# Kernel tuning notes

Measured on AMD Instinct MI355X. Metric: run time of the kernel, lower is better.

The kernel has to match this reference:

```python
import jax, jax.numpy as jnp
import numpy as np
import math

B, S, D, H = 4, 1024, 1024, 16

def setup_inputs() -> dict:
    key = jax.random.key(0)
    ks = jax.random.split(key, 9)
    Q = jax.random.normal(ks[0], (B, S, D), dtype=jnp.float32)
    K = jax.random.normal(ks[1], (B, S, D), dtype=jnp.float32)
    V = jax.random.normal(ks[2], (B, S, D), dtype=jnp.float32)
    mask = jax.random.randint(ks[3], (B, 1, S, S), 0, 2, dtype=jnp.int32)
    # keep the diagonal unmasked so no causal row is fully -inf (avoids NaN softmax rows)
    eye = jnp.eye(S, dtype=jnp.int32)[None, None]
    mask = jnp.maximum(mask, eye)
    sc = 1.0 / math.sqrt(D)
    Wq = jax.random.normal(ks[4], (D, D), dtype=jnp.float32) * sc
    Wk = jax.random.normal(ks[5], (D, D), dtype=jnp.float32) * sc
    Wv = jax.random.normal(ks[6], (D, D), dtype=jnp.float32) * sc
    Wo = jax.random.normal(ks[7], (D, D), dtype=jnp.float32) * sc
    bo = jnp.zeros((D,), dtype=jnp.float32)
    return {"Q": Q, "K": K, "V": V, "mask": mask,
            "Wq": Wq, "Wk": Wk, "Wv": Wv, "Wo": Wo, "bo": bo, "heads": H}


def reference(Q, K, V, mask, Wq, Wk, Wv, Wo, bo, heads):
    b, s, d = Q.shape
    dk = d // heads
    # QKV projections (bias-free) and head split: [B,S,D] -> [B,H,S,dk]
    def split_heads(x, W):
        return (x @ W).reshape(b, s, heads, dk).transpose(0, 2, 1, 3)
    q = split_heads(Q, Wq)
    k = split_heads(K, Wk)
    v = split_heads(V, Wv)
    # raw scores [B,H,S,S]
    attn = jnp.einsum('bhqd,bhkd->bhqk', q, k) / jnp.sqrt(jnp.float32(dk))
    # multiplicative padding mask
    attn = attn * mask.astype(attn.dtype)
    # sequential=True: torch.tril zeroes the strict upper triangle
    causal = jnp.tril(jnp.ones((s, s), dtype=attn.dtype))
    attn = attn * causal
    # the module's quirk: exact zeros become -inf before softmax
    attn = jnp.where(attn == 0, -jnp.inf, attn)
    scores = jax.nn.softmax(attn, axis=-1)  # dropout is identity in eval / p=0
    ctx = jnp.einsum('bhqk,bhkd->bhqd', scores, v)
    concat = ctx.transpose(0, 2, 1, 3).reshape(b, s, d)
    return concat @ Wo + bo
```

## Files before the change

### kernel.cpp

```cpp
#include <hip/hip_runtime.h>

#define DEV __device__ __forceinline__

typedef __bf16 bf16x8 __attribute__((ext_vector_type(8)));
typedef float f32x4 __attribute__((ext_vector_type(4)));
typedef unsigned short u16x8 __attribute__((ext_vector_type(8)));
typedef unsigned int u32;
typedef unsigned long long u64;

DEV unsigned short f2bf(float f) {
  union { float f; unsigned int u; } v; v.f = f;
  unsigned int r = v.u + 0x7fffu + ((v.u >> 16) & 1u);
  return (unsigned short)(r >> 16);
}

DEV int swz(int row, int kbyte) { return row * 128 + (kbyte ^ ((row & 7) << 4)); }

DEV void gload16(const void* g, void* l) {
  __builtin_amdgcn_global_load_lds(
      (const __attribute__((address_space(1))) unsigned int*)g,
      (__attribute__((address_space(3))) unsigned int*)l, 16, 0, 0);
}

__global__ __launch_bounds__(256) void pack_mask_k(const int* __restrict__ mask,
                                                   u32* __restrict__ bits) {
  int e = blockIdx.x * 256 + threadIdx.x;
  int k = e & 1023, q = (e >> 10) & 1023;
  int m = (mask[e] != 0) && (k <= q);
  unsigned long long b = __ballot(m);
  int lane = threadIdx.x & 63;
  if (lane == 0)       bits[e >> 5] = (u32)b;
  else if (lane == 32) bits[e >> 5] = (u32)(b >> 32);
}

__global__ __launch_bounds__(256) void xcast_k(
    const float* __restrict__ Qx, const float* __restrict__ Kx, const float* __restrict__ Vx,
    unsigned short* __restrict__ qp, unsigned short* __restrict__ kp,
    unsigned short* __restrict__ vp) {
  int z = blockIdx.y;
  const float* X = z == 0 ? Qx : z == 1 ? Kx : Vx;
  unsigned short* P = z == 0 ? qp : z == 1 ? kp : vp;
  int tile = blockIdx.x;
  int mb = tile >> 4, kt = tile & 15;
  int t = threadIdx.x;
  size_t tb = (size_t)tile * 16384;
  #pragma unroll
  for (int i = 0; i < 4; i++) {
    int idx = i * 256 + t;
    int r = idx >> 3, j = idx & 7;
    int c0 = ((j * 16) ^ ((r & 7) << 4)) >> 1;
    const float* src = X + (size_t)(mb * 128 + r) * 1024 + kt * 64 + c0;
    f32x4 a = *(const f32x4*)src;
    f32x4 bq = *(const f32x4*)(src + 4);
    u16x8 o;
    o[0] = f2bf(a[0]); o[1] = f2bf(a[1]); o[2] = f2bf(a[2]); o[3] = f2bf(a[3]);
    o[4] = f2bf(bq[0]); o[5] = f2bf(bq[1]); o[6] = f2bf(bq[2]); o[7] = f2bf(bq[3]);
    *(u16x8*)((char*)P + tb + (size_t)idx * 16) = o;
  }
}

__global__ __launch_bounds__(256) void wtrans_k(
    const float* __restrict__ W0, const float* __restrict__ W1,
    const float* __restrict__ W2, const float* __restrict__ W3,
    unsigned short* __restrict__ O0, unsigned short* __restrict__ O1,
    unsigned short* __restrict__ O2, unsigned short* __restrict__ O3) {
  const float* W = blockIdx.z == 0 ? W0 : blockIdx.z == 1 ? W1 : blockIdx.z == 2 ? W2 : W3;
  unsigned short* O = blockIdx.z == 0 ? O0 : blockIdx.z == 1 ? O1 : blockIdx.z == 2 ? O2 : O3;
  __shared__ float tile[32][33];
  int tx = threadIdx.x, ty = threadIdx.y;
  int x0 = blockIdx.x * 32, y0 = blockIdx.y * 32;
  #pragma unroll
  for (int i = 0; i < 4; i++)
    tile[ty + i * 8][tx] = W[(size_t)(y0 + ty + i * 8) * 1024 + x0 + tx];
  __syncthreads();
  #pragma unroll
  for (int i = 0; i < 4; i++) {
    int n = x0 + ty + i * 8, k = y0 + tx;
    size_t a = (size_t)((n >> 7) * 16 + (k >> 6)) * 16384 + swz(n & 127, (k & 63) * 2);
    *(unsigned short*)((char*)O + a) = f2bf(tile[tx][ty + i * 8]);
  }
}

__global__ __launch_bounds__(256) void proj_gemm_k(
    const unsigned short* __restrict__ Qp, const unsigned short* __restrict__ Kp,
    const unsigned short* __restrict__ Vp,
    const unsigned short* __restrict__ Wtq, const unsigned short* __restrict__ Wtk,
    const unsigned short* __restrict__ Wtv,
    unsigned short* __restrict__ qo, unsigned short* __restrict__ ko,
    unsigned short* __restrict__ vo) {
  int z = blockIdx.z;
  const unsigned short* Ap = z == 0 ? Qp : z == 1 ? Kp : Vp;
  const unsigned short* Bp = z == 0 ? Wtq : z == 1 ? Wtk : Wtv;
  unsigned short* out = z == 0 ? qo : z == 1 ? ko : vo;

  __shared__ __align__(16) unsigned short As[8192];
  __shared__ __align__(16) unsigned short Bs[8192];

  int t = threadIdx.x, w = t >> 6, lane = t & 63;
  int wm = (w >> 1) * 64, wn = (w & 1) * 64;
  int rl = lane & 15, kgrp = lane >> 4;

  f32x4 acc[4][4];
  #pragma unroll
  for (int m = 0; m < 4; m++)
    #pragma unroll
    for (int n = 0; n < 4; n++)
      #pragma unroll
      for (int r = 0; r < 4; r++) acc[m][n][r] = 0.f;

  for (int kt = 0; kt < 16; kt++) {
    __syncthreads();
    const char* ab = (const char*)Ap + (size_t)(blockIdx.x * 16 + kt) * 16384 + w * 1024 + lane * 16;
    const char* bb = (const char*)Bp + (size_t)(blockIdx.y * 16 + kt) * 16384 + w * 1024 + lane * 16;
    char* al = (char*)As + w * 1024;
    char* bl = (char*)Bs + w * 1024;
    #pragma unroll
    for (int i = 0; i < 4; i++) {
      gload16(ab + i * 4096, al + i * 4096);
      gload16(bb + i * 4096, bl + i * 4096);
    }
    __syncthreads();
    #pragma unroll
    for (int kk = 0; kk < 2; kk++) {
      bf16x8 af[4], bfr[4];
      #pragma unroll
      for (int m = 0; m < 4; m++)
        af[m] = *(const bf16x8*)((const char*)As + swz(wm + m * 16 + rl, kk * 64 + kgrp * 16));
      #pragma unroll
      for (int n = 0; n < 4; n++)
        bfr[n] = *(const bf16x8*)((const char*)Bs + swz(wn + n * 16 + rl, kk * 64 + kgrp * 16));
      #pragma unroll
      for (int m = 0; m < 4; m++)
        #pragma unroll
        for (int n = 0; n < 4; n++)
          acc[m][n] = __builtin_amdgcn_mfma_f32_16x16x32_bf16(af[m], bfr[n], acc[m][n], 0, 0, 0);
    }
  }
  int m0 = blockIdx.x * 128, n0 = blockIdx.y * 128;
  #pragma unroll
  for (int m = 0; m < 4; m++)
    #pragma unroll
    for (int n = 0; n < 4; n++)
      #pragma unroll
      for (int r = 0; r < 4; r++) {
        int grow = m0 + wm + m * 16 + kgrp * 4 + r;
        int gcol = n0 + wn + n * 16 + rl;
        int b = grow >> 10, s = grow & 1023;
        int h = gcol >> 6, d = gcol & 63;
        unsigned short val = f2bf(acc[m][n][r]);
        if (z == 0) {
          out[(size_t)((b * 16 + h) * 1024 + s) * 64 + d] = val;
        } else if (z == 1) {
          *(unsigned short*)((char*)out +
            (size_t)((b * 16 + h) * 16 + (s >> 6)) * 8192 + swz(s & 63, d * 2)) = val;
        } else {
          *(unsigned short*)((char*)out +
            (size_t)((b * 16 + h) * 16 + (s >> 6)) * 8192 + swz(d, (s & 63) * 2)) = val;
        }
      }
}

__global__ __launch_bounds__(256) void attn_k(
    const unsigned short* __restrict__ qg, const unsigned short* __restrict__ kp,
    const unsigned short* __restrict__ vp, const u32* __restrict__ mbits,
    unsigned short* __restrict__ ccp) {
  int p = blockIdx.x;
  int bh = blockIdx.y;
  int b = bh >> 4, h = bh & 15;
  int t = threadIdx.x, w = t >> 6, lane = t & 63;
  int rl = lane & 15, kgrp = lane >> 4;

  const int qtA = p, qtB = 15 - p, J = qtB + 1;
  const int q0s[2] = {qtA * 64, qtB * 64};

  __shared__ __align__(16) unsigned short Ks[2][4096];
  __shared__ __align__(16) unsigned short Vs[2][4096];
  __shared__ __align__(16) unsigned short Ps[4][1024];

  const size_t qoff = (size_t)bh * 65536;
  const char* kbase = (const char*)kp + (size_t)bh * 131072;
  const char* vbase = (const char*)vp + (size_t)bh * 131072;

  bf16x8 qa[2][2];
  #pragma unroll
  for (int tl = 0; tl < 2; tl++) {
    int row = q0s[tl] + w * 16 + rl;
    #pragma unroll
    for (int kk = 0; kk < 2; kk++)
      qa[tl][kk] = *(const bf16x8*)(qg + qoff + (size_t)row * 64 + kk * 32 + kgrp * 8);
  }

  {
    const char* kg = kbase + w * 1024 + lane * 16;
    const char* vg = vbase + w * 1024 + lane * 16;
    char* kl = (char*)Ks[0] + w * 1024;
    char* vl = (char*)Vs[0] + w * 1024;
    gload16(kg, kl); gload16(kg + 4096, kl + 4096);
    gload16(vg, vl); gload16(vg + 4096, vl + 4096);
  }

  float lsum[2][4];
  f32x4 acc[2][4];
  #pragma unroll
  for (int tl = 0; tl < 2; tl++)
    #pragma unroll
    for (int r = 0; r < 4; r++) {
      lsum[tl][r] = 0.f;
      #pragma unroll
      for (int d = 0; d < 4; d++) acc[tl][d][r] = 0.f;
    }

  for (int j = 0; j < J; j++) {
    __syncthreads();
    if (j + 1 < J) {
      int nb = (j + 1) & 1;
      const char* kg = kbase + (size_t)(j + 1) * 8192 + w * 1024 + lane * 16;
      const char* vg = vbase + (size_t)(j + 1) * 8192 + w * 1024 + lane * 16;
      char* kl = (char*)Ks[nb] + w * 1024;
      char* vl = (char*)Vs[nb] + w * 1024;
      gload16(kg, kl); gload16(kg + 4096, kl + 4096);
      gload16(vg, vl); gload16(vg + 4096, vl + 4096);
    }
    const char* Kb = (const char*)Ks[j & 1];
    const char* Vb = (const char*)Vs[j & 1];

    #pragma unroll
    for (int tl = 1; tl >= 0; tl--) {
      if (tl == 0 && j > qtA) continue;
      const int q0 = q0s[tl];
      f32x4 sc[4];
      #pragma unroll
      for (int n = 0; n < 4; n++) {
        f32x4 z4;
        #pragma unroll
        for (int r = 0; r < 4; r++) z4[r] = 0.f;
        bf16x8 kb0 = *(const bf16x8*)(Kb + swz(n * 16 + rl, 0 * 64 + kgrp * 16));
        bf16x8 kb1 = *(const bf16x8*)(Kb + swz(n * 16 + rl, 1 * 64 + kgrp * 16));
        z4 = __builtin_amdgcn_mfma_f32_16x16x32_bf16(qa[tl][0], kb0, z4, 0, 0, 0);
        sc[n] = __builtin_amdgcn_mfma_f32_16x16x32_bf16(qa[tl][1], kb1, z4, 0, 0, 0);
      }
      u32 b0[4], b1[4];
      #pragma unroll
      for (int r = 0; r < 4; r++) {
        int qrow = q0 + w * 16 + kgrp * 4 + r;
        u64 mw = *(const u64*)(mbits + ((size_t)(b * 1024 + qrow) * 32 + j * 2));
        b0[r] = (u32)mw >> rl;
        b1[r] = (u32)(mw >> 32) >> rl;
      }
      const float C = 0.18033688011112042f;
      float pe[4][4];
      #pragma unroll
      for (int n = 0; n < 4; n++) {
        #pragma unroll
        for (int r = 0; r < 4; r++) {
          u32 bit = ((n & 2) ? b1[r] : b0[r]) >> ((n & 1) << 4);
          float ex = exp2f(sc[n][r] * C);
          bool keep = (bit & 1u) && (sc[n][r] != 0.f);
          pe[n][r] = keep ? ex : 0.f;
        }
      }
      #pragma unroll
      for (int r = 0; r < 4; r++)
        lsum[tl][r] += (pe[0][r] + pe[1][r]) + (pe[2][r] + pe[3][r]);
      unsigned short* pb = &Ps[w][0];
      #pragma unroll
      for (int n = 0; n < 4; n++) {
        int col = n * 16 + rl;
        #pragma unroll
        for (int r = 0; r < 4; r++)
          *(unsigned short*)((char*)pb + swz(kgrp * 4 + r, col * 2)) = f2bf(pe[n][r]);
      }
      bf16x8 pa[2];
      #pragma unroll
      for (int kk = 0; kk < 2; kk++)
        pa[kk] = *(const bf16x8*)((const char*)pb + swz(rl, kk * 64 + kgrp * 16));
      #pragma unroll
      for (int d = 0; d < 4; d++) {
        bf16x8 vb0 = *(const bf16x8*)(Vb + swz(d * 16 + rl, 0 * 64 + kgrp * 16));
        bf16x8 vb1 = *(const bf16x8*)(Vb + swz(d * 16 + rl, 1 * 64 + kgrp * 16));
        acc[tl][d] = __builtin_amdgcn_mfma_f32_16x16x32_bf16(pa[0], vb0, acc[tl][d], 0, 0, 0);
        acc[tl][d] = __builtin_amdgcn_mfma_f32_16x16x32_bf16(pa[1], vb1, acc[tl][d], 0, 0, 0);
      }
    }
  }
  #pragma unroll
  for (int tl = 0; tl < 2; tl++)
    #pragma unroll
    for (int r = 0; r < 4; r++) {
      float l = lsum[tl][r];
      l += __shfl_xor(l, 1); l += __shfl_xor(l, 2);
      l += __shfl_xor(l, 4); l += __shfl_xor(l, 8);
      float linv = 1.f / l;
      int srow = q0s[tl] + w * 16 + kgrp * 4 + r;
      int grow = b * 1024 + srow;
      char* tbase = (char*)ccp + (size_t)((grow >> 7) * 16 + h) * 16384;
      int rr = grow & 127;
      #pragma unroll
      for (int d = 0; d < 4; d++)
        *(unsigned short*)(tbase + swz(rr, (d * 16 + rl) * 2)) = f2bf(acc[tl][d][r] * linv);
    }
}

__global__ __launch_bounds__(256) void out_gemm_k(
    const unsigned short* __restrict__ Ap, const unsigned short* __restrict__ Bp,
    const float* __restrict__ bias, float* __restrict__ out) {
  __shared__ __align__(16) unsigned short As[8192];
  __shared__ __align__(16) unsigned short Bs[8192];

  int t = threadIdx.x, w = t >> 6, lane = t & 63;
  int wm = (w >> 1) * 64, wn = (w & 1) * 64;
  int rl = lane & 15, kgrp = lane >> 4;

  f32x4 acc[4][4];
  #pragma unroll
  for (int m = 0; m < 4; m++)
    #pragma unroll
    for (int n = 0; n < 4; n++)
      #pragma unroll
      for (int r = 0; r < 4; r++) acc[m][n][r] = 0.f;

  for (int kt = 0; kt < 16; kt++) {
    __syncthreads();
    const char* ab = (const char*)Ap + (size_t)(blockIdx.x * 16 + kt) * 16384 + w * 1024 + lane * 16;
    const char* bb = (const char*)Bp + (size_t)(blockIdx.y * 16 + kt) * 16384 + w * 1024 + lane * 16;
    char* al = (char*)As + w * 1024;
    char* bl = (char*)Bs + w * 1024;
    #pragma unroll
    for (int i = 0; i < 4; i++) {
      gload16(ab + i * 4096, al + i * 4096);
      gload16(bb + i * 4096, bl + i * 4096);
    }
    __syncthreads();
    #pragma unroll
    for (int kk = 0; kk < 2; kk++) {
      bf16x8 af[4], bfr[4];
      #pragma unroll
      for (int m = 0; m < 4; m++)
        af[m] = *(const bf16x8*)((const char*)As + swz(wm + m * 16 + rl, kk * 64 + kgrp * 16));
      #pragma unroll
      for (int n = 0; n < 4; n++)
        bfr[n] = *(const bf16x8*)((const char*)Bs + swz(wn + n * 16 + rl, kk * 64 + kgrp * 16));
      #pragma unroll
      for (int m = 0; m < 4; m++)
        #pragma unroll
        for (int n = 0; n < 4; n++)
          acc[m][n] = __builtin_amdgcn_mfma_f32_16x16x32_bf16(af[m], bfr[n], acc[m][n], 0, 0, 0);
    }
  }
  int m0 = blockIdx.x * 128, n0 = blockIdx.y * 128;
  #pragma unroll
  for (int m = 0; m < 4; m++)
    #pragma unroll
    for (int n = 0; n < 4; n++)
      #pragma unroll
      for (int r = 0; r < 4; r++) {
        int grow = m0 + wm + m * 16 + kgrp * 4 + r;
        int gcol = n0 + wn + n * 16 + rl;
        out[(size_t)grow * 1024 + gcol] = acc[m][n][r] + bias[gcol];
      }
}

extern "C" void kernel_launch(void* const* d_in, const int* in_sizes, int n_in,
                              void* d_out, int out_size, void* d_ws, size_t ws_size,
                              hipStream_t stream) {
  const float* Q  = (const float*)d_in[0];
  const float* K  = (const float*)d_in[1];
  const float* V  = (const float*)d_in[2];
  const int* mask = (const int*)d_in[3];
  const float* Wq = (const float*)d_in[4];
  const float* Wk = (const float*)d_in[5];
  const float* Wv = (const float*)d_in[6];
  const float* Wo = (const float*)d_in[7];
  const float* bo = (const float*)d_in[8];
  float* out = (float*)d_out;

  char* ws = (char*)d_ws;
  unsigned short* xq  = (unsigned short*)(ws);
  unsigned short* xk  = (unsigned short*)(ws + (8u  << 20));
  unsigned short* xv  = (unsigned short*)(ws + (16u << 20));
  unsigned short* ccp = (unsigned short*)(ws);
  unsigned short* qb  = (unsigned short*)(ws + (24u << 20));
  unsigned short* kpk = (unsigned short*)(ws + (32u << 20));
  unsigned short* vpk = (unsigned short*)(ws + (40u << 20));
  unsigned short* wqt = (unsigned short*)(ws + (48u << 20));
  unsigned short* wkt = (unsigned short*)(ws + (50u << 20));
  unsigned short* wvt = (unsigned short*)(ws + (52u << 20));
  unsigned short* wot = (unsigned short*)(ws + (54u << 20));
  u32*            mb  = (u32*)(ws + (56u << 20));

  pack_mask_k<<<16384, 256, 0, stream>>>(mask, mb);
  xcast_k<<<dim3(512, 3), 256, 0, stream>>>(Q, K, V, xq, xk, xv);
  wtrans_k<<<dim3(32, 32, 4), dim3(32, 8), 0, stream>>>(Wq, Wk, Wv, Wo, wqt, wkt, wvt, wot);
  proj_gemm_k<<<dim3(32, 8, 3), 256, 0, stream>>>(xq, xk, xv, wqt, wkt, wvt, qb, kpk, vpk);
  attn_k<<<dim3(8, 64), 256, 0, stream>>>(qb, kpk, vpk, mb, ccp);
  out_gemm_k<<<dim3(32, 8), 256, 0, stream>>>(ccp, wot, bo, out);
}
```

Baseline: 238.6 us.

## Fuse prep kernels into one launch and split attention into per-tile blocks

Merges mask packing, activation casting and weight transposition into a single prep kernel dispatched by block index, removing two kernel launches. The attention kernel stops pairing a short and a long query tile per block and instead launches one block per query tile, heaviest first. This doubles parallelism and lowers per-block register state, at the cost of less even per-block work and re-loading K/V per tile.

New measurement: 249.0 us. 1.04x slower.

```diff
diff --git a/kernel.cpp b/kernel.cpp
--- a/kernel.cpp
+++ b/kernel.cpp
@@ -22,62 +22,62 @@
       (__attribute__((address_space(3))) unsigned int*)l, 16, 0, 0);
 }
 
-__global__ __launch_bounds__(256) void pack_mask_k(const int* __restrict__ mask,
-                                                   u32* __restrict__ bits) {
-  int e = blockIdx.x * 256 + threadIdx.x;
-  int k = e & 1023, q = (e >> 10) & 1023;
-  int m = (mask[e] != 0) && (k <= q);
-  unsigned long long b = __ballot(m);
-  int lane = threadIdx.x & 63;
-  if (lane == 0)       bits[e >> 5] = (u32)b;
-  else if (lane == 32) bits[e >> 5] = (u32)(b >> 32);
-}
-
-__global__ __launch_bounds__(256) void xcast_k(
+__global__ __launch_bounds__(256) void prep_k(
+    const int* __restrict__ mask, u32* __restrict__ bits,
     const float* __restrict__ Qx, const float* __restrict__ Kx, const float* __restrict__ Vx,
     unsigned short* __restrict__ qp, unsigned short* __restrict__ kp,
-    unsigned short* __restrict__ vp) {
-  int z = blockIdx.y;
-  const float* X = z == 0 ? Qx : z == 1 ? Kx : Vx;
-  unsigned short* P = z == 0 ? qp : z == 1 ? kp : vp;
-  int tile = blockIdx.x;
-  int mb = tile >> 4, kt = tile & 15;
-  int t = threadIdx.x;
-  size_t tb = (size_t)tile * 16384;
-  #pragma unroll
-  for (int i = 0; i < 4; i++) {
-    int idx = i * 256 + t;
-    int r = idx >> 3, j = idx & 7;
-    int c0 = ((j * 16) ^ ((r & 7) << 4)) >> 1;
-    const float* src = X + (size_t)(mb * 128 + r) * 1024 + kt * 64 + c0;
-    f32x4 a = *(const f32x4*)src;
-    f32x4 bq = *(const f32x4*)(src + 4);
-    u16x8 o;
-    o[0] = f2bf(a[0]); o[1] = f2bf(a[1]); o[2] = f2bf(a[2]); o[3] = f2bf(a[3]);
-    o[4] = f2bf(bq[0]); o[5] = f2bf(bq[1]); o[6] = f2bf(bq[2]); o[7] = f2bf(bq[3]);
-    *(u16x8*)((char*)P + tb + (size_t)idx * 16) = o;
-  }
-}
-
-__global__ __launch_bounds__(256) void wtrans_k(
+    unsigned short* __restrict__ vp,
     const float* __restrict__ W0, const float* __restrict__ W1,
     const float* __restrict__ W2, const float* __restrict__ W3,
     unsigned short* __restrict__ O0, unsigned short* __restrict__ O1,
     unsigned short* __restrict__ O2, unsigned short* __restrict__ O3) {
-  const float* W = blockIdx.z == 0 ? W0 : blockIdx.z == 1 ? W1 : blockIdx.z == 2 ? W2 : W3;
-  unsigned short* O = blockIdx.z == 0 ? O0 : blockIdx.z == 1 ? O1 : blockIdx.z == 2 ? O2 : O3;
   __shared__ float tile[32][33];
-  int tx = threadIdx.x, ty = threadIdx.y;
-  int x0 = blockIdx.x * 32, y0 = blockIdx.y * 32;
-  #pragma unroll
-  for (int i = 0; i < 4; i++)
-    tile[ty + i * 8][tx] = W[(size_t)(y0 + ty + i * 8) * 1024 + x0 + tx];
-  __syncthreads();
-  #pragma unroll
-  for (int i = 0; i < 4; i++) {
-    int n = x0 + ty + i * 8, k = y0 + tx;
-    size_t a = (size_t)((n >> 7) * 16 + (k >> 6)) * 16384 + swz(n & 127, (k & 63) * 2);
-    *(unsigned short*)((char*)O + a) = f2bf(tile[tx][ty + i * 8]);
+  int bid = blockIdx.x, t = threadIdx.x;
+  if (bid < 16384) {
+    int e = bid * 256 + t;
+    int k = e & 1023, q = (e >> 10) & 1023;
+    int m = (mask[e] != 0) && (k <= q);
+    unsigned long long b = __ballot(m);
+    int lane = t & 63;
+    if (lane == 0)       bits[e >> 5] = (u32)b;
+    else if (lane == 32) bits[e >> 5] = (u32)(b >> 32);
+  } else if (bid < 17920) {
+    int r2 = bid - 16384;
+    int z = r2 >> 9, tl = r2 & 511;
+    const float* X = z == 0 ? Qx : z == 1 ? Kx : Vx;
+    unsigned short* P = z == 0 ? qp : z == 1 ? kp : vp;
+    int mb = tl >> 4, kt = tl & 15;
+    size_t tb = (size_t)tl * 16384;
+    #pragma unroll
+    for (int i = 0; i < 4; i++) {
+      int idx = i * 256 + t;
+      int r = idx >> 3, j = idx & 7;
+      int c0 = ((j * 16) ^ ((r & 7) << 4)) >> 1;
+      const float* src = X + (size_t)(mb * 128 + r) * 1024 + kt * 64 + c0;
+      f32x4 a = *(const f32x4*)src;
+      f32x4 bq = *(const f32x4*)(src + 4);
+      u16x8 o;
+      o[0] = f2bf(a[0]); o[1] = f2bf(a[1]); o[2] = f2bf(a[2]); o[3] = f2bf(a[3]);
+      o[4] = f2bf(bq[0]); o[5] = f2bf(bq[1]); o[6] = f2bf(bq[2]); o[7] = f2bf(bq[3]);
+      *(u16x8*)((char*)P + tb + (size_t)idx * 16) = o;
+    }
+  } else {
+    int r2 = bid - 17920;
+    int z = r2 >> 10, rem = r2 & 1023;
+    const float* W = z == 0 ? W0 : z == 1 ? W1 : z == 2 ? W2 : W3;
+    unsigned short* O = z == 0 ? O0 : z == 1 ? O1 : z == 2 ? O2 : O3;
+    int tx = t & 31, ty = t >> 5;
+    int x0 = (rem & 31) * 32, y0 = (rem >> 5) * 32;
+    #pragma unroll
+    for (int i = 0; i < 4; i++)
+      tile[ty + i * 8][tx] = W[(size_t)(y0 + ty + i * 8) * 1024 + x0 + tx];
+    __syncthreads();
+    #pragma unroll
+    for (int i = 0; i < 4; i++) {
+      int n = x0 + ty + i * 8, k = y0 + tx;
+      size_t a = (size_t)((n >> 7) * 16 + (k >> 6)) * 16384 + swz(n & 127, (k & 63) * 2);
+      *(unsigned short*)((char*)O + a) = f2bf(tile[tx][ty + i * 8]);
+    }
   }
 }
 
@@ -164,14 +164,14 @@
     const unsigned short* __restrict__ qg, const unsigned short* __restrict__ kp,
     const unsigned short* __restrict__ vp, const u32* __restrict__ mbits,
     unsigned short* __restrict__ ccp) {
-  int p = blockIdx.x;
+  int qt = 15 - (int)blockIdx.x;
   int bh = blockIdx.y;
   int b = bh >> 4, h = bh & 15;
   int t = threadIdx.x, w = t >> 6, lane = t & 63;
   int rl = lane & 15, kgrp = lane >> 4;
 
-  const int qtA = p, qtB = 15 - p, J = qtB + 1;
-  const int q0s[2] = {qtA * 64, qtB * 64};
+  const int J = qt + 1;
+  const int q0 = qt * 64;
 
   __shared__ __align__(16) unsigned short Ks[2][4096];
   __shared__ __align__(16) unsigned short Vs[2][4096];
@@ -181,13 +181,12 @@
   const char* kbase = (const char*)kp + (size_t)bh * 131072;
   const char* vbase = (const char*)vp + (size_t)bh * 131072;
 
-  bf16x8 qa[2][2];
-  #pragma unroll
-  for (int tl = 0; tl < 2; tl++) {
-    int row = q0s[tl] + w * 16 + rl;
+  bf16x8 qa[2];
+  {
+    int row = q0 + w * 16 + rl;
     #pragma unroll
     for (int kk = 0; kk < 2; kk++)
-      qa[tl][kk] = *(const bf16x8*)(qg + qoff + (size_t)row * 64 + kk * 32 + kgrp * 8);
+      qa[kk] = *(const bf16x8*)(qg + qoff + (size_t)row * 64 + kk * 32 + kgrp * 8);
   }
 
   {
@@ -199,16 +198,14 @@
     gload16(vg, vl); gload16(vg + 4096, vl + 4096);
   }
 
-  float lsum[2][4];
-  f32x4 acc[2][4];
-  #pragma unroll
-  for (int tl = 0; tl < 2; tl++)
-    #pragma unroll
-    for (int r = 0; r < 4; r++) {
-      lsum[tl][r] = 0.f;
-      #pragma unroll
-      for (int d = 0; d < 4; d++) acc[tl][d][r] = 0.f;
-    }
+  float lsum[4];
+  f32x4 acc[4];
+  #pragma unroll
+  for (int r = 0; r < 4; r++) {
+    lsum[r] = 0.f;
+    #pragma unroll
+    for (int d = 0; d < 4; d++) acc[d][r] = 0.f;
+  }
 
   for (int j = 0; j < J; j++) {
     __syncthreads();
@@ -224,81 +221,74 @@
     const char* Kb = (const char*)Ks[j & 1];
     const char* Vb = (const char*)Vs[j & 1];
 
-    #pragma unroll
-    for (int tl = 1; tl >= 0; tl--) {
-      if (tl == 0 && j > qtA) continue;
-      const int q0 = q0s[tl];
-      f32x4 sc[4];
-      #pragma unroll
-      for (int n = 0; n < 4; n++) {
-        f32x4 z4;
-        #pragma unroll
-        for (int r = 0; r < 4; r++) z4[r] = 0.f;
-        bf16x8 kb0 = *(const bf16x8*)(Kb + swz(n * 16 + rl, 0 * 64 + kgrp * 16));
-        bf16x8 kb1 = *(const bf16x8*)(Kb + swz(n * 16 + rl, 1 * 64 + kgrp * 16));
-        z4 = __builtin_amdgcn_mfma_f32_16x16x32_bf16(qa[tl][0], kb0, z4, 0, 0, 0);
-        sc[n] = __builtin_amdgcn_mfma_f32_16x16x32_bf16(qa[tl][1], kb1, z4, 0, 0, 0);
+    f32x4 sc[4];
+    #pragma unroll
+    for (int n = 0; n < 4; n++) {
+      f32x4 z4;
+      #pragma unroll
+      for (int r = 0; r < 4; r++) z4[r] = 0.f;
+      bf16x8 kb0 = *(const bf16x8*)(Kb + swz(n * 16 + rl, 0 * 64 + kgrp * 16));
+      bf16x8 kb1 = *(const bf16x8*)(Kb + swz(n * 16 + rl, 1 * 64 + kgrp * 16));
+      z4 = __builtin_amdgcn_mfma_f32_16x16x32_bf16(qa[0], kb0, z4, 0, 0, 0);
+      sc[n] = __builtin_amdgcn_mfma_f32_16x16x32_bf16(qa[1], kb1, z4, 0, 0, 0);
+    }
+    u32 b0[4], b1[4];
+    #pragma unroll
+    for (int r = 0; r < 4; r++) {
+      int qrow = q0 + w * 16 + kgrp * 4 + r;
+      u64 mw = *(const u64*)(mbits + ((size_t)(b * 1024 + qrow) * 32 + j * 2));
+      b0[r] = (u32)mw >> rl;
+      b1[r] = (u32)(mw >> 32) >> rl;
+    }
+    const float C = 0.18033688011112042f;
+    float pe[4][4];
+    #pragma unroll
+    for (int n = 0; n < 4; n++) {
+      #pragma unroll
+      for (int r = 0; r < 4; r++) {
+        u32 bit = ((n & 2) ? b1[r] : b0[r]) >> ((n & 1) << 4);
+        float ex = exp2f(sc[n][r] * C);
+        bool keep = (bit & 1u) && (sc[n][r] != 0.f);
+        pe[n][r] = keep ? ex : 0.f;
       }
-      u32 b0[4], b1[4];
-      #pragma unroll
-      for (int r = 0; r < 4; r++) {
-        int qrow = q0 + w * 16 + kgrp * 4 + r;
-        u64 mw = *(const u64*)(mbits + ((size_t)(b * 1024 + qrow) * 32 + j * 2));
-        b0[r] = (u32)mw >> rl;
-        b1[r] = (u32)(mw >> 32) >> rl;
-      }
-      const float C = 0.18033688011112042f;
-      float pe[4][4];
-      #pragma unroll
-      for (int n = 0; n < 4; n++) {
-        #pragma unroll
-        for (int r = 0; r < 4; r++) {
-          u32 bit = ((n & 2) ? b1[r] : b0[r]) >> ((n & 1) << 4);
-          float ex = exp2f(sc[n][r] * C);
-          bool keep = (bit & 1u) && (sc[n][r] != 0.f);
-          pe[n][r] = keep ? ex : 0.f;
-        }
-      }
+    }
+    #pragma unroll
+    for (int r = 0; r < 4; r++)
+      lsum[r] += (pe[0][r] + pe[1][r]) + (pe[2][r] + pe[3][r]);
+    unsigned short* pb = &Ps[w][0];
+    #pragma unroll
+    for (int n = 0; n < 4; n++) {
+      int col = n * 16 + rl;
       #pragma unroll
       for (int r = 0; r < 4; r++)
-        lsum[tl][r] += (pe[0][r] + pe[1][r]) + (pe[2][r] + pe[3][r]);
-      unsigned short* pb = &Ps[w][0];
-      #pragma unroll
-      for (int n = 0; n < 4; n++) {
-        int col = n * 16 + rl;
-        #pragma unroll
-        for (int r = 0; r < 4; r++)
-          *(unsigned short*)((char*)pb + swz(kgrp * 4 + r, col * 2)) = f2bf(pe[n][r]);
-      }
-      bf16x8 pa[2];
-      #pragma unroll
-      for (int kk = 0; kk < 2; kk++)
-        pa[kk] = *(const bf16x8*)((const char*)pb + swz(rl, kk * 64 + kgrp * 16));
-      #pragma unroll
-      for (int d = 0; d < 4; d++) {
-        bf16x8 vb0 = *(const bf16x8*)(Vb + swz(d * 16 + rl, 0 * 64 + kgrp * 16));
-        bf16x8 vb1 = *(const bf16x8*)(Vb + swz(d * 16 + rl, 1 * 64 + kgrp * 16));
-        acc[tl][d] = __builtin_amdgcn_mfma_f32_16x16x32_bf16(pa[0], vb0, acc[tl][d], 0, 0, 0);
-        acc[tl][d] = __builtin_amdgcn_mfma_f32_16x16x32_bf16(pa[1], vb1, acc[tl][d], 0, 0, 0);
-      }
-    }
-  }
-  #pragma unroll
-  for (int tl = 0; tl < 2; tl++)
-    #pragma unroll
-    for (int r = 0; r < 4; r++) {
-      float l = lsum[tl][r];
-      l += __shfl_xor(l, 1); l += __shfl_xor(l, 2);
-      l += __shfl_xor(l, 4); l += __shfl_xor(l, 8);
-      float linv = 1.f / l;
-      int srow = q0s[tl] + w * 16 + kgrp * 4 + r;
-      int grow = b * 1024 + srow;
-      char* tbase = (char*)ccp + (size_t)((grow >> 7) * 16 + h) * 16384;
-      int rr = grow & 127;
-      #pragma unroll
-      for (int d = 0; d < 4; d++)
-        *(unsigned short*)(tbase + swz(rr, (d * 16 + rl) * 2)) = f2bf(acc[tl][d][r] * linv);
-    }
+        *(unsigned short*)((char*)pb + swz(kgrp * 4 + r, col * 2)) = f2bf(pe[n][r]);
+    }
+    bf16x8 pa[2];
+    #pragma unroll
+    for (int kk = 0; kk < 2; kk++)
+      pa[kk] = *(const bf16x8*)((const char*)pb + swz(rl, kk * 64 + kgrp * 16));
+    #pragma unroll
+    for (int d = 0; d < 4; d++) {
+      bf16x8 vb0 = *(const bf16x8*)(Vb + swz(d * 16 + rl, 0 * 64 + kgrp * 16));
+      bf16x8 vb1 = *(const bf16x8*)(Vb + swz(d * 16 + rl, 1 * 64 + kgrp * 16));
+      acc[d] = __builtin_amdgcn_mfma_f32_16x16x32_bf16(pa[0], vb0, acc[d], 0, 0, 0);
+      acc[d] = __builtin_amdgcn_mfma_f32_16x16x32_bf16(pa[1], vb1, acc[d], 0, 0, 0);
+    }
+  }
+  #pragma unroll
+  for (int r = 0; r < 4; r++) {
+    float l = lsum[r];
+    l += __shfl_xor(l, 1); l += __shfl_xor(l, 2);
+    l += __shfl_xor(l, 4); l += __shfl_xor(l, 8);
+    float linv = 1.f / l;
+    int srow = q0 + w * 16 + kgrp * 4 + r;
+    int grow = b * 1024 + srow;
+    char* tbase = (char*)ccp + (size_t)((grow >> 7) * 16 + h) * 16384;
+    int rr = grow & 127;
+    #pragma unroll
+    for (int d = 0; d < 4; d++)
+      *(unsigned short*)(tbase + swz(rr, (d * 16 + rl) * 2)) = f2bf(acc[d][r] * linv);
+  }
 }
 
 __global__ __launch_bounds__(256) void out_gemm_k(
@@ -388,10 +378,9 @@
   unsigned short* wot = (unsigned short*)(ws + (54u << 20));
   u32*            mb  = (u32*)(ws + (56u << 20));
 
-  pack_mask_k<<<16384, 256, 0, stream>>>(mask, mb);
-  xcast_k<<<dim3(512, 3), 256, 0, stream>>>(Q, K, V, xq, xk, xv);
-  wtrans_k<<<dim3(32, 32, 4), dim3(32, 8), 0, stream>>>(Wq, Wk, Wv, Wo, wqt, wkt, wvt, wot);
+  prep_k<<<22016, 256, 0, stream>>>(mask, mb, Q, K, V, xq, xk, xv,
+                                    Wq, Wk, Wv, Wo, wqt, wkt, wvt, wot);
   proj_gemm_k<<<dim3(32, 8, 3), 256, 0, stream>>>(xq, xk, xv, wqt, wkt, wvt, qb, kpk, vpk);
-  attn_k<<<dim3(8, 64), 256, 0, stream>>>(qb, kpk, vpk, mb, ccp);
+  attn_k<<<dim3(16, 64), 256, 0, stream>>>(qb, kpk, vpk, mb, ccp);
   out_gemm_k<<<dim3(32, 8), 256, 0, stream>>>(ccp, wot, bo, out);
 }
```
